# Kernel optimization log

Measured on AMD Instinct MI355X. Metric: run time of the kernel, lower is better.

## Reference

```python
import jax, jax.numpy as jnp
import numpy as np

B, D, U = 64, 256, 256

def setup_inputs() -> dict:
    key = jax.random.key(0)
    ks = jax.random.split(key, 16)
    init_mu = 0.05
    inputs = jax.random.normal(ks[0], (B, D), jnp.float32)
    prev_state = 0.1 * jax.random.normal(ks[1], (B, U), jnp.float32)
    A = jax.random.normal(ks[2], (B, U, U), jnp.float32)
    # symmetric, diagonally boosted covariance-like state
    Sigma_state = 0.01 * (A + jnp.swapaxes(A, 1, 2)) + 0.1 * jnp.eye(U, dtype=jnp.float32)
    def w(k, shape):
        return init_mu * jax.random.normal(k, shape, jnp.float32)
    def s(k):
        return jax.random.uniform(k, (U,), jnp.float32, -4.5, -2.2)
    return {
        'inputs': inputs, 'prev_state': prev_state, 'Sigma_state': Sigma_state,
        'U_z': w(ks[3], (D, U)), 'uz_sigma': s(ks[4]), 'W_z': w(ks[5], (U, U)), 'wz_sigma': s(ks[6]),
        'U_r': w(ks[7], (D, U)), 'ur_sigma': s(ks[8]), 'W_r': w(ks[9], (U, U)), 'wr_sigma': s(ks[10]),
        'U_h': w(ks[11], (D, U)), 'uh_sigma': s(ks[12]), 'W_h': w(ks[13], (U, U)), 'wh_sigma': s(ks[14]),
    }

def _outer(a, b):  # [B,u],[B,u] -> [B,u,u]
    return a[:, :, None] * b[:, None, :]

def _quad(W, S):  # W^T @ S @ W, S is [B,u,u]
    return jnp.matmul(jnp.matmul(W.T, S), W)

def _x_sigma_w(x, sv):  # ||x||^2 * diag(softplus sigma)
    return jnp.sum(x * x, axis=1)[:, None, None] * jnp.diag(sv)

def _tr_sigma_w(S, sv):  # trace(S) * diag(softplus sigma)
    return jnp.trace(S, axis1=1, axis2=2)[:, None, None] * jnp.diag(sv)

def _hadamard_sigma(S1, S2, m1, m2):
    # S1*S2 + diag(m1) S2 diag(m1) + diag(m2) S1 diag(m2) as elementwise/broadcast
    return S1 * S2 + _outer(m1, m1) * S2 + _outer(m2, m2) * S1

def reference(inputs, prev_state, Sigma_state, U_z, uz_sigma, W_z, wz_sigma,
              U_r, ur_sigma, W_r, wr_sigma, U_h, uh_sigma, W_h, wh_sigma):
    sp = jax.nn.softplus
    # --- z gate ---
    az = inputs @ U_z + prev_state @ W_z
    z = jax.nn.sigmoid(az)
    gz = z * (1.0 - z)  # d sigmoid
    Sz = (_quad(W_z, Sigma_state) + _x_sigma_w(prev_state, sp(wz_sigma))
          + _tr_sigma_w(Sigma_state, sp(wz_sigma)) + _x_sigma_w(inputs, sp(uz_sigma)))
    Sigma_out_z = Sz * _outer(gz, gz)
    # --- r gate ---
    ar = inputs @ U_r + prev_state @ W_r
    r = jax.nn.sigmoid(ar)
    gr = r * (1.0 - r)
    Sr = (_quad(W_r, Sigma_state) + _x_sigma_w(prev_state, sp(wr_sigma))
          + _tr_sigma_w(Sigma_state, sp(wr_sigma)) + _x_sigma_w(inputs, sp(ur_sigma)))
    Sigma_out_r = Sr * _outer(gr, gr)
    # --- h candidate ---
    g_in = prev_state * r
    ah = inputs @ U_h + g_in @ W_h
    h = jnp.tanh(ah)
    gh = 1.0 - h * h  # d tanh
    sigma_g = _hadamard_sigma(Sigma_state, Sigma_out_r, prev_state, r)
    Sh = (_quad(W_h, sigma_g) + _x_sigma_w(g_in, sp(wh_sigma))
          + _tr_sigma_w(sigma_g, sp(wh_sigma)) + _x_sigma_w(inputs, sp(uh_sigma)))
    Sigma_out_h = Sh * _outer(gh, gh)
    # --- output combination ---
    mu_out = z * prev_state + (1.0 - z) * h
    sigma_a = _hadamard_sigma(Sigma_out_z, Sigma_state, z, prev_state)
    sigma_b = _hadamard_sigma(Sigma_out_z, Sigma_out_h, 1.0 - z, h)
    Sigma_out = (sigma_a + sigma_b
                 - Sigma_out_z * _outer(prev_state, h)
                 - Sigma_out_z * _outer(h, prev_state))
    Sigma_out = jnp.where(jnp.isnan(Sigma_out) | jnp.isinf(Sigma_out),
                          jnp.zeros_like(Sigma_out), Sigma_out)
    eye = jnp.eye(Sigma_out.shape[-1], dtype=Sigma_out.dtype)
    d = jnp.abs(jnp.diagonal(Sigma_out, axis1=1, axis2=2))
    Sigma_out = Sigma_out * (1.0 - eye) + d[:, :, None] * eye
    return mu_out, Sigma_out
```

## Files before the change

kernel.cpp:

```cpp
#include <hip/hip_runtime.h>
#include <math.h>

#define UDIM 256
#define BATCH 64
#define MATN 65536
#define PITCH 280

typedef __bf16 bf16x8 __attribute__((ext_vector_type(8)));
typedef float  f32x4  __attribute__((ext_vector_type(4)));

__device__ __forceinline__ float softplusf(float x) { return log1pf(expf(x)); }
__device__ __forceinline__ float sigmoidf_(float x) { return 1.f/(1.f+expf(-x)); }

__device__ __forceinline__ bf16x8 frag_load(const __bf16* base, int rt, int kt, int lane) {
  return *(const bf16x8*)(base + (((size_t)(rt*8 + kt))*64 + lane)*8);
}

__device__ __forceinline__ bf16x8 cvt8(const float* p) {
  const float4 f0 = *(const float4*)p;
  const float4 f1 = *(const float4*)(p + 4);
  bf16x8 v;
  v[0]=(__bf16)f0.x; v[1]=(__bf16)f0.y; v[2]=(__bf16)f0.z; v[3]=(__bf16)f0.w;
  v[4]=(__bf16)f1.x; v[5]=(__bf16)f1.y; v[6]=(__bf16)f1.z; v[7]=(__bf16)f1.w;
  return v;
}

#define MFMA16 __builtin_amdgcn_mfma_f32_16x16x32_bf16

__global__ __launch_bounds__(256) void prep_all(
    const float* __restrict__ Uz, const float* __restrict__ Wz,
    const float* __restrict__ Ur, const float* __restrict__ Wr,
    const float* __restrict__ Uh, const float* __restrict__ Wh,
    __bf16* __restrict__ Fw_z, __bf16* __restrict__ Fw_r,
    __bf16* __restrict__ Fu_h, __bf16* __restrict__ Fw_h,
    const float* __restrict__ S, const float* __restrict__ x,
    const float* __restrict__ prev, float* __restrict__ scal,
    __bf16* __restrict__ Sf,
    float* __restrict__ zb, float* __restrict__ rb,
    float* __restrict__ gzb, float* __restrict__ grb,
    float* __restrict__ gin)
{
  const int bid = blockIdx.x;
  const int t = threadIdx.x;
  const int w = t >> 6, l = t & 63, r = l & 15, q = l >> 4;

  __shared__ __align__(16) unsigned char LDSU[16896];

  if (bid < 1024) {
    const int c = bid;
    const int bx = c & 3, by = (c >> 2) & 3, b = c >> 4;
    const size_t sb = (size_t)b * MATN;
#pragma unroll
    for (int ss = 0; ss < 2; ++ss) {
      const int s = t + ss*256;
      const int chunk = s >> 6, lane = s & 63;
      const int rt_l = chunk >> 1, kt_l = chunk & 1;
      const int row = by*64 + rt_l*16 + (lane & 15);
      const int col = bx*64 + kt_l*32 + (lane >> 4)*8;
      const bf16x8 v = cvt8(S + sb + (size_t)row*UDIM + col);
      *(bf16x8*)(Sf + sb + (((size_t)((by*4 + rt_l)*8 + bx*2 + kt_l))*64 + lane)*8) = v;
    }
    return;
  }

  if (bid < 1088) {
    const int u3 = bid - 1024;
    const int mat = u3 >> 4, tl = u3 & 15;
    const int n0 = (tl & 3)*64, k0 = (tl >> 2)*64;
    const float* W; __bf16* F;
    switch (mat) {
      case 0: W = Wz; F = Fw_z; break;  case 1: W = Wr; F = Fw_r; break;
      case 2: W = Uh; F = Fu_h; break;  default: W = Wh; F = Fw_h; break;
    }
    float (*tile)[65] = (float (*)[65])LDSU;
    const int tx = t & 15, ty = t >> 4;
#pragma unroll
    for (int rr = 0; rr < 4; ++rr) {
      const int row = ty*4 + rr;
      const float4 f = *(const float4*)(W + (size_t)(k0 + row)*UDIM + n0 + tx*4);
      tile[row][tx*4+0] = f.x; tile[row][tx*4+1] = f.y;
      tile[row][tx*4+2] = f.z; tile[row][tx*4+3] = f.w;
    }
    __syncthreads();
#pragma unroll
    for (int ss = 0; ss < 2; ++ss) {
      const int s = t + ss*256;
      const int rt_l = s >> 7, kt_l = (s >> 6) & 1, lane = s & 63;
      const int nl = rt_l*16 + (lane & 15), kb = kt_l*32 + (lane >> 4)*8;
      __align__(16) __bf16 tmp[8];
#pragma unroll
      for (int e = 0; e < 8; ++e) tmp[e] = (__bf16)tile[kb + e][nl];
      *(uint4*)(F + (((size_t)((((n0 >> 4) + rt_l)*8) + (k0 >> 5) + kt_l))*64 + lane)*8)
          = *(const uint4*)tmp;
    }
    return;
  }

  if (bid < 1104) {
    const int blk = bid - 1088;
    const int b0 = blk*4 + (t >> 6);
    const float4 xv = *(const float4*)(x + b0*UDIM + l*4);
    float s0 = xv.x*xv.x + xv.y*xv.y + xv.z*xv.z + xv.w*xv.w;
    const float4 pv = *(const float4*)(prev + b0*UDIM + l*4);
    float s1 = pv.x*pv.x + pv.y*pv.y + pv.z*pv.z + pv.w*pv.w;
    float s2 = 0.f;
#pragma unroll
    for (int e = 0; e < 4; ++e)
      s2 += S[(size_t)b0*MATN + (size_t)(l*4 + e)*257];
    for (int off = 32; off; off >>= 1) {
      s0 += __shfl_down(s0, off);
      s1 += __shfl_down(s1, off);
      s2 += __shfl_down(s2, off);
    }
    if (l == 0) { scal[b0] = s0; scal[64 + b0] = s1; scal[128 + b0] = s2; }
    return;
  }

  {
    const int u2 = bid - 1104;
    const int g = u2 >> 4, un = u2 & 15;
    const int n0 = un * 16;
    const float* Um = g ? Ur : Uz;
    const float* Wm = g ? Wr : Wz;
    __bf16 (*Ut)[16][264] = (__bf16 (*)[16][264])LDSU;
    {
      float uv[16], wv[16];
      const float* ur_ = Um + (size_t)t*UDIM + n0;
      const float* wr_ = Wm + (size_t)t*UDIM + n0;
#pragma unroll
      for (int p4 = 0; p4 < 4; ++p4) {
        *(float4*)&uv[p4*4] = *(const float4*)(ur_ + p4*4);
        *(float4*)&wv[p4*4] = *(const float4*)(wr_ + p4*4);
      }
#pragma unroll
      for (int e = 0; e < 16; ++e) {
        Ut[0][e][t] = (__bf16)uv[e];
        Ut[1][e][t] = (__bf16)wv[e];
      }
    }
    __syncthreads();

    const int mrow = w*16 + r;
    f32x4 acc = {};
#pragma unroll
    for (int ks = 0; ks < 16; ++ks) {
      const int k0 = ks*32;
      const float* asrc;
      int src, koff;
      if (k0 < 256) { asrc = x    + (size_t)mrow*UDIM + k0         + q*8; src = 0; koff = k0; }
      else          { asrc = prev + (size_t)mrow*UDIM + (k0 - 256) + q*8; src = 1; koff = k0 - 256; }
      const bf16x8 af = cvt8(asrc);
      const bf16x8 bv = *(const bf16x8*)&Ut[src][r][koff + q*8];
      acc = MFMA16(af, bv, acc, 0, 0, 0);
    }
    const int n = n0 + r;
    if (g == 0) {
#pragma unroll
      for (int v = 0; v < 4; ++v) {
        const int m = w*16 + q*4 + v;
        const float zv = sigmoidf_(acc[v]);
        zb[m*UDIM + n]  = zv;
        gzb[m*UDIM + n] = zv * (1.f - zv);
      }
    } else {
      float ggp[4];
#pragma unroll
      for (int v = 0; v < 4; ++v) {
        const int m = w*16 + q*4 + v;
        const float rv = sigmoidf_(acc[v]);
        const float pv = prev[m*UDIM + n];
        const float g2 = pv * rv;
        rb[m*UDIM + n]  = rv;
        grb[m*UDIM + n] = rv * (1.f - rv);
        gin[m*UDIM + n] = g2;
        ggp[v] = g2 * g2;
      }
#pragma unroll
      for (int s2 = 1; s2 < 16; s2 <<= 1)
#pragma unroll
        for (int v = 0; v < 4; ++v) ggp[v] += __shfl_xor(ggp[v], s2);
      if (r == 0)
#pragma unroll
        for (int v = 0; v < 4; ++v)
          atomicAdd(&scal[192 + w*16 + q*4 + v], ggp[v]);
    }
  }
}

__global__ __launch_bounds__(256, 4) void quad_zr_gh(
    const float* __restrict__ S, const __bf16* __restrict__ Sf,
    const float* __restrict__ prev,
    const float* __restrict__ rb, const float* __restrict__ gzb,
    const float* __restrict__ grb,
    const float* __restrict__ wz_s, const float* __restrict__ uz_s,
    const float* __restrict__ wr_s, const float* __restrict__ ur_s,
    const __bf16* __restrict__ Fw_z, const __bf16* __restrict__ Fw_r,
    float* __restrict__ scal, __bf16* __restrict__ Szb, __bf16* __restrict__ G,
    const float* __restrict__ x, const float* __restrict__ gin,
    const float* __restrict__ zb,
    const __bf16* __restrict__ Fu_h, const __bf16* __restrict__ Fw_h,
    float* __restrict__ hb, float* __restrict__ ghb, float* __restrict__ mu_out)
{
  const int bid = blockIdx.x;
  const int t = threadIdx.x, w = t >> 6, l = t & 63, r = l & 15, q = l >> 4;

  if (bid < 4) {
    const int jt = bid;
    const int mrow = w*16 + r;
    f32x4 acc[4] = {};
#pragma unroll
    for (int ks = 0; ks < 16; ++ks) {
      const int k0 = ks*32;
      const float* asrc; const __bf16* B; int kk;
      if (k0 < 256) { asrc = x   + (size_t)mrow*UDIM + k0         + q*8; B = Fu_h; kk = k0; }
      else          { asrc = gin + (size_t)mrow*UDIM + (k0 - 256) + q*8; B = Fw_h; kk = k0 - 256; }
      const bf16x8 af = cvt8(asrc);
#pragma unroll
      for (int ni = 0; ni < 4; ++ni) {
        const bf16x8 bv = frag_load(B, jt*4 + ni, kk >> 5, l);
        acc[ni] = MFMA16(af, bv, acc[ni], 0, 0, 0);
      }
    }
#pragma unroll
    for (int ni = 0; ni < 4; ++ni) {
      const int n = jt*64 + ni*16 + r;
#pragma unroll
      for (int v = 0; v < 4; ++v) {
        const int m = w*16 + q*4 + v;
        const float hv = tanhf(acc[ni][v]);
        const float zv = zb[m*UDIM + n];
        hb[m*UDIM + n]  = hv;
        ghb[m*UDIM + n] = 1.f - hv*hv;
        mu_out[m*UDIM + n] = zv * prev[m*UDIM + n] + (1.f - zv) * hv;
      }
    }
    return;
  }

  const int id = bid - 4;
  const int s = id >> 6, b = id & 63;
  const size_t sb = (size_t)b * MATN;
  const __bf16* Sfb = Sf + sb;

  __shared__ __align__(16) __bf16 T[2*16*PITCH];
  __bf16* Tz = T;
  __bf16* Tr = T + 16*PITCH;

  f32x4 az[4] = {}, ar[4] = {};
#pragma unroll
  for (int kp = 0; kp < 4; ++kp) {
    bf16x8 wzf[2], wrf[2], sv[2][4];
#pragma unroll
    for (int u = 0; u < 2; ++u) {
      const int kt = kp*2 + u;
      wzf[u] = frag_load(Fw_z, s, kt, l);
      wrf[u] = frag_load(Fw_r, s, kt, l);
#pragma unroll
      for (int ct = 0; ct < 4; ++ct) sv[u][ct] = frag_load(Sfb, w*4 + ct, kt, l);
    }
#pragma unroll
    for (int u = 0; u < 2; ++u)
#pragma unroll
      for (int ct = 0; ct < 4; ++ct) {
        az[ct] = MFMA16(wzf[u], sv[u][ct], az[ct], 0, 0, 0);
        ar[ct] = MFMA16(wrf[u], sv[u][ct], ar[ct], 0, 0, 0);
      }
  }
#pragma unroll
  for (int ct = 0; ct < 4; ++ct)
#pragma unroll
    for (int v = 0; v < 4; ++v) {
      Tz[(q*4 + v)*PITCH + w*64 + ct*16 + r] = (__bf16)az[ct][v];
      Tr[(q*4 + v)*PITCH + w*64 + ct*16 + r] = (__bf16)ar[ct][v];
    }
  __syncthreads();

  const int ib = s*16 + q*4;
  const f32x4 gz4 = *(const f32x4*)(gzb + b*UDIM + ib);
  const f32x4 gr4 = *(const f32x4*)(grb + b*UDIM + ib);
  const f32x4 pp4 = *(const f32x4*)(prev + b*UDIM + ib);
  const f32x4 rr4 = *(const f32x4*)(rb + b*UDIM + ib);
  float Sv[16];
#pragma unroll
  for (int ct = 0; ct < 4; ++ct)
#pragma unroll
    for (int v = 0; v < 4; ++v)
      Sv[ct*4 + v] = S[sb + (size_t)(ib + v)*UDIM + (w*4 + ct)*16 + r];
  const float xx = scal[b];
  const float dscal = scal[64 + b] + scal[128 + b];

  f32x4 qz[4] = {}, qr[4] = {};
#pragma unroll
  for (int kt = 0; kt < 8; ++kt) {
    bf16x8 bwz[4], bwr[4];
#pragma unroll
    for (int ct = 0; ct < 4; ++ct) {
      bwz[ct] = frag_load(Fw_z, w*4 + ct, kt, l);
      bwr[ct] = frag_load(Fw_r, w*4 + ct, kt, l);
    }
    const bf16x8 atz = *(const bf16x8*)&Tz[r*PITCH + kt*32 + q*8];
    const bf16x8 atr = *(const bf16x8*)&Tr[r*PITCH + kt*32 + q*8];
#pragma unroll
    for (int ct = 0; ct < 4; ++ct) {
      qz[ct] = MFMA16(atz, bwz[ct], qz[ct], 0, 0, 0);
      qr[ct] = MFMA16(atr, bwr[ct], qr[ct], 0, 0, 0);
    }
  }

  {
    __align__(16) __bf16 o16[16];
#pragma unroll
    for (int ct = 0; ct < 4; ++ct) {
      const int j = (w*4 + ct)*16 + r;
      const float gj = gzb[b*UDIM + j];
#pragma unroll
      for (int v = 0; v < 4; ++v) {
        const int i = ib + v;
        float qv = qz[ct][v];
        if (i == j) qv += dscal*softplusf(wz_s[i]) + xx*softplusf(uz_s[i]);
        o16[ct*4 + v] = (__bf16)(qv * gz4[v] * gj);
      }
    }
    __bf16* dst = Szb + ((size_t)(b*16 + s)*256 + t)*16;
    *(uint4*)dst       = *(const uint4*)&o16[0];
    *(uint4*)(dst + 8) = *(const uint4*)&o16[8];
  }

  {
    float gvals[16];
    float trg = 0.f;
#pragma unroll
    for (int ct = 0; ct < 4; ++ct) {
      const int j = (w*4 + ct)*16 + r;
      const float gj = grb[b*UDIM + j];
      const float pj = prev[b*UDIM + j];
      const float rj = rb[b*UDIM + j];
#pragma unroll
      for (int v = 0; v < 4; ++v) {
        const int i = ib + v;
        float qv = qr[ct][v];
        if (i == j) qv += dscal*softplusf(wr_s[i]) + xx*softplusf(ur_s[i]);
        const float Sg = qv * gr4[v] * gj;
        const float sv = Sv[ct*4 + v];
        const float go = Sg*(sv + pp4[v]*pj) + rr4[v]*rj*sv;
        gvals[ct*4 + v] = go;
        if (i == j) trg += go;
      }
    }
    if (trg != 0.f) atomicAdd(&scal[256 + b], trg);

    __syncthreads();
#pragma unroll
    for (int ct = 0; ct < 4; ++ct)
#pragma unroll
      for (int v = 0; v < 4; ++v)
        Tr[(q*4 + v)*PITCH + w*64 + ct*16 + r] = (__bf16)gvals[ct*4 + v];
    __syncthreads();
#pragma unroll
    for (int ee = 0; ee < 2; ++ee) {
      const int e = t + ee*256;
      const int kt = e >> 6, le = e & 63;
      const uint4 vv = *(const uint4*)&Tr[(le & 15)*PITCH + kt*32 + (le >> 4)*8];
      *(uint4*)(G + sb + (((size_t)(s*8 + kt))*64 + le)*8) = vv;
    }
  }
}

__global__ __launch_bounds__(256, 4) void quad_h(
    const float* __restrict__ S, const __bf16* __restrict__ Szb,
    const float* __restrict__ prev, const float* __restrict__ zb,
    const float* __restrict__ hb, const float* __restrict__ ghb,
    const float* __restrict__ wh_s, const float* __restrict__ uh_s,
    const __bf16* __restrict__ Fw_h, const __bf16* __restrict__ G,
    const float* __restrict__ scal, float* __restrict__ out_sig)
{
  const int bid = blockIdx.x;
  const int s = bid >> 6, b = bid & 63;
  const size_t sb = (size_t)b * MATN;
  const int t = threadIdx.x, w = t >> 6, l = t & 63, r = l & 15, q = l >> 4;
  const __bf16* Gb = G + sb;

  __shared__ __align__(16) __bf16 Th[16*PITCH];

  f32x4 ah[4] = {};
#pragma unroll
  for (int kp = 0; kp < 4; ++kp) {
    bf16x8 af[2], bv[2][4];
#pragma unroll
    for (int u = 0; u < 2; ++u) {
      const int kt = kp*2 + u;
      af[u] = frag_load(Fw_h, s, kt, l);
#pragma unroll
      for (int ct = 0; ct < 4; ++ct) bv[u][ct] = frag_load(Gb, w*4 + ct, kt, l);
    }
#pragma unroll
    for (int u = 0; u < 2; ++u)
#pragma unroll
      for (int ct = 0; ct < 4; ++ct)
        ah[ct] = MFMA16(af[u], bv[u][ct], ah[ct], 0, 0, 0);
  }
#pragma unroll
  for (int ct = 0; ct < 4; ++ct)
#pragma unroll
    for (int v = 0; v < 4; ++v)
      Th[(q*4 + v)*PITCH + w*64 + ct*16 + r] = (__bf16)ah[ct][v];
  __syncthreads();

  const int ib = s*16 + q*4;
  const __bf16* szp = Szb + ((size_t)(b*16 + s)*256 + t)*16;
  __align__(16) __bf16 sz16[16];
  *(uint4*)&sz16[0] = *(const uint4*)szp;
  *(uint4*)&sz16[8] = *(const uint4*)(szp + 8);
  const f32x4 g4 = *(const f32x4*)(ghb + b*UDIM + ib);
  const f32x4 p4 = *(const f32x4*)(prev + b*UDIM + ib);
  const f32x4 z4 = *(const f32x4*)(zb + b*UDIM + ib);
  const f32x4 h4 = *(const f32x4*)(hb + b*UDIM + ib);
  float Sv[16], gjv[4], pjv[4], zjv[4], hjv[4];
#pragma unroll
  for (int ct = 0; ct < 4; ++ct) {
    const int j = (w*4 + ct)*16 + r;
    gjv[ct] = ghb[b*UDIM + j];
    pjv[ct] = prev[b*UDIM + j];
    zjv[ct] = zb[b*UDIM + j];
    hjv[ct] = hb[b*UDIM + j];
#pragma unroll
    for (int v = 0; v < 4; ++v)
      Sv[ct*4 + v] = S[sb + (size_t)(ib + v)*UDIM + j];
  }
  const float xx = scal[b];
  const float dscal = scal[192 + b] + scal[256 + b];

  f32x4 qh[4] = {};
#pragma unroll
  for (int kt = 0; kt < 8; ++kt) {
    bf16x8 bw[4];
#pragma unroll
    for (int ct = 0; ct < 4; ++ct) bw[ct] = frag_load(Fw_h, w*4 + ct, kt, l);
    const bf16x8 at = *(const bf16x8*)&Th[r*PITCH + kt*32 + q*8];
#pragma unroll
    for (int ct = 0; ct < 4; ++ct)
      qh[ct] = MFMA16(at, bw[ct], qh[ct], 0, 0, 0);
  }

#pragma unroll
  for (int ct = 0; ct < 4; ++ct) {
    const int j = (w*4 + ct)*16 + r;
#pragma unroll
    for (int v = 0; v < 4; ++v) {
      const int i = ib + v;
      float qv = qh[ct][v];
      if (i == j) qv += dscal*softplusf(wh_s[i]) + xx*softplusf(uh_s[i]);
      const float Sg = qv * g4[v] * gjv[ct];
      const float sv = Sv[ct*4 + v];
      const float sz = (float)sz16[ct*4 + v];
      float val = sv*(sz + z4[v]*zjv[ct])
                + sz*(p4[v] - h4[v])*(pjv[ct] - hjv[ct])
                + Sg*(sz + (1.f - z4[v])*(1.f - zjv[ct]));
      if (!isfinite(val)) val = 0.f;
      if (i == j) val = fabsf(val);
      out_sig[sb + (size_t)i*UDIM + j] = val;
    }
  }
}

extern "C" void kernel_launch(void* const* d_in, const int* in_sizes, int n_in,
                              void* d_out, int out_size, void* d_ws, size_t ws_size,
                              hipStream_t stream) {
  const float* x    = (const float*)d_in[0];
  const float* prev = (const float*)d_in[1];
  const float* S    = (const float*)d_in[2];
  const float* Uz   = (const float*)d_in[3];
  const float* uz_s = (const float*)d_in[4];
  const float* Wz   = (const float*)d_in[5];
  const float* wz_s = (const float*)d_in[6];
  const float* Ur   = (const float*)d_in[7];
  const float* ur_s = (const float*)d_in[8];
  const float* Wr   = (const float*)d_in[9];
  const float* wr_s = (const float*)d_in[10];
  const float* Uh   = (const float*)d_in[11];
  const float* uh_s = (const float*)d_in[12];
  const float* Wh   = (const float*)d_in[13];
  const float* wh_s = (const float*)d_in[14];

  float* out_mu  = (float*)d_out;
  float* out_sig = out_mu + BATCH*UDIM;

  float* ws   = (float*)d_ws;
  float* zb   = ws;
  float* rb   = zb  + BATCH*UDIM;
  float* gzb  = rb  + BATCH*UDIM;
  float* grb  = gzb + BATCH*UDIM;
  float* gin  = grb + BATCH*UDIM;
  float* hb   = gin + BATCH*UDIM;
  float* ghb  = hb  + BATCH*UDIM;
  float* scal = ghb + BATCH*UDIM;
  __bf16* bws  = (__bf16*)(scal + 512);
  __bf16* Fw_z = bws;
  __bf16* Fw_r = Fw_z + MATN;
  __bf16* Fu_h = Fw_r + MATN;
  __bf16* Fw_h = Fu_h + MATN;
  const size_t BIG = (size_t)BATCH * MATN;
  __bf16* Szb = Fw_h + MATN;
  __bf16* G   = Szb + BIG;
  __bf16* Sf  = G + BIG;

  (void)hipMemsetAsync(scal, 0, 512*sizeof(float), stream);

  prep_all<<<dim3(1136), 256, 0, stream>>>(Uz, Wz, Ur, Wr, Uh, Wh,
      Fw_z, Fw_r, Fu_h, Fw_h, S, x, prev, scal, Sf,
      zb, rb, gzb, grb, gin);
  quad_zr_gh<<<dim3(1028), 256, 0, stream>>>(S, Sf, prev, rb, gzb, grb,
      wz_s, uz_s, wr_s, ur_s, Fw_z, Fw_r, scal, Szb, G,
      x, gin, zb, Fu_h, Fw_h, hb, ghb, out_mu);
  quad_h<<<dim3(1024), 256, 0, stream>>>(S, Szb, prev, zb, hb, ghb,
      wh_s, uh_s, Fw_h, G, scal, out_sig);
}
```

Before: 164.2 us.

## Fuse z/r and h quadratic kernels with per-batch atomic counter barrier

Merges the z/r-gate quadratic kernel and the h-gate quadratic kernel into one launch. The 16 row-slab blocks of each batch synchronise through a global atomic counter spin-wait, and the h-candidate GEMM work is spread across 16 blocks that signal a separate counter. This keeps the z-gate covariance slab in registers instead of writing and re-reading an Szb bf16 buffer, and reuses the already loaded S values and prev. It removes one kernel launch and a large intermediate round trip, but relies on all 1024 blocks being co-resident to avoid deadlock and adds spin-wait stalls.

```diff
diff --git a/kernel.cpp b/kernel.cpp
--- a/kernel.cpp
+++ b/kernel.cpp
@@ -187,64 +187,67 @@
   }
 }
 
-__global__ __launch_bounds__(256, 4) void quad_zr_gh(
+__global__ __launch_bounds__(256, 4) void quad_all(
     const float* __restrict__ S, const __bf16* __restrict__ Sf,
     const float* __restrict__ prev,
     const float* __restrict__ rb, const float* __restrict__ gzb,
     const float* __restrict__ grb,
     const float* __restrict__ wz_s, const float* __restrict__ uz_s,
     const float* __restrict__ wr_s, const float* __restrict__ ur_s,
+    const float* __restrict__ wh_s, const float* __restrict__ uh_s,
     const __bf16* __restrict__ Fw_z, const __bf16* __restrict__ Fw_r,
-    float* __restrict__ scal, __bf16* __restrict__ Szb, __bf16* __restrict__ G,
+    const __bf16* __restrict__ Fu_h, const __bf16* __restrict__ Fw_h,
+    float* __restrict__ scal, unsigned int* __restrict__ cnt,
+    __bf16* __restrict__ G,
     const float* __restrict__ x, const float* __restrict__ gin,
     const float* __restrict__ zb,
-    const __bf16* __restrict__ Fu_h, const __bf16* __restrict__ Fw_h,
-    float* __restrict__ hb, float* __restrict__ ghb, float* __restrict__ mu_out)
+    float* __restrict__ hb, float* __restrict__ ghb,
+    float* __restrict__ mu_out, float* __restrict__ out_sig)
 {
   const int bid = blockIdx.x;
+  const int s = bid >> 6, b = bid & 63;
   const int t = threadIdx.x, w = t >> 6, l = t & 63, r = l & 15, q = l >> 4;
-
-  if (bid < 4) {
-    const int jt = bid;
-    const int mrow = w*16 + r;
-    f32x4 acc[4] = {};
-#pragma unroll
-    for (int ks = 0; ks < 16; ++ks) {
-      const int k0 = ks*32;
-      const float* asrc; const __bf16* B; int kk;
-      if (k0 < 256) { asrc = x   + (size_t)mrow*UDIM + k0         + q*8; B = Fu_h; kk = k0; }
-      else          { asrc = gin + (size_t)mrow*UDIM + (k0 - 256) + q*8; B = Fw_h; kk = k0 - 256; }
-      const bf16x8 af = cvt8(asrc);
-#pragma unroll
-      for (int ni = 0; ni < 4; ++ni) {
-        const bf16x8 bv = frag_load(B, jt*4 + ni, kk >> 5, l);
-        acc[ni] = MFMA16(af, bv, acc[ni], 0, 0, 0);
-      }
-    }
-#pragma unroll
-    for (int ni = 0; ni < 4; ++ni) {
-      const int n = jt*64 + ni*16 + r;
-#pragma unroll
-      for (int v = 0; v < 4; ++v) {
-        const int m = w*16 + q*4 + v;
-        const float hv = tanhf(acc[ni][v]);
-        const float zv = zb[m*UDIM + n];
-        hb[m*UDIM + n]  = hv;
-        ghb[m*UDIM + n] = 1.f - hv*hv;
-        mu_out[m*UDIM + n] = zv * prev[m*UDIM + n] + (1.f - zv) * hv;
-      }
-    }
-    return;
-  }
-
-  const int id = bid - 4;
-  const int s = id >> 6, b = id & 63;
   const size_t sb = (size_t)b * MATN;
   const __bf16* Sfb = Sf + sb;
 
   __shared__ __align__(16) __bf16 T[2*16*PITCH];
   __bf16* Tz = T;
   __bf16* Tr = T + 16*PITCH;
+
+  if (s == 15 && b >= 48) {
+    const int un = b - 48;
+    const int mrow = w*16 + r;
+    f32x4 acc = {};
+#pragma unroll
+    for (int kq = 0; kq < 4; ++kq) {
+      bf16x8 af[4], bv[4];
+#pragma unroll
+      for (int u = 0; u < 4; ++u) {
+        const int k0 = (kq*4 + u)*32;
+        if (k0 < 256) {
+          af[u] = cvt8(x   + (size_t)mrow*UDIM + k0 + q*8);
+          bv[u] = frag_load(Fu_h, un, k0 >> 5, l);
+        } else {
+          af[u] = cvt8(gin + (size_t)mrow*UDIM + (k0 - 256) + q*8);
+          bv[u] = frag_load(Fw_h, un, (k0 - 256) >> 5, l);
+        }
+      }
+#pragma unroll
+      for (int u = 0; u < 4; ++u) acc = MFMA16(af[u], bv[u], acc, 0, 0, 0);
+    }
+    const int n = un*16 + r;
+#pragma unroll
+    for (int v = 0; v < 4; ++v) {
+      const int m = w*16 + q*4 + v;
+      const float hv = tanhf(acc[v]);
+      const float zv = zb[m*UDIM + n];
+      hb[m*UDIM + n]  = hv;
+      ghb[m*UDIM + n] = 1.f - hv*hv;
+      mu_out[m*UDIM + n] = zv * prev[m*UDIM + n] + (1.f - zv) * hv;
+    }
+    __syncthreads();
+    if (t == 0) { __threadfence(); atomicAdd(&cnt[64], 1u); }
+  }
 
   f32x4 az[4] = {}, ar[4] = {};
 #pragma unroll
@@ -280,12 +283,15 @@
   const f32x4 gr4 = *(const f32x4*)(grb + b*UDIM + ib);
   const f32x4 pp4 = *(const f32x4*)(prev + b*UDIM + ib);
   const f32x4 rr4 = *(const f32x4*)(rb + b*UDIM + ib);
-  float Sv[16];
-#pragma unroll
-  for (int ct = 0; ct < 4; ++ct)
+  float Sv[16], pjv[4];
+#pragma unroll
+  for (int ct = 0; ct < 4; ++ct) {
+    const int j = (w*4 + ct)*16 + r;
+    pjv[ct] = prev[b*UDIM + j];
 #pragma unroll
     for (int v = 0; v < 4; ++v)
-      Sv[ct*4 + v] = S[sb + (size_t)(ib + v)*UDIM + (w*4 + ct)*16 + r];
+      Sv[ct*4 + v] = S[sb + (size_t)(ib + v)*UDIM + j];
+  }
   const float xx = scal[b];
   const float dscal = scal[64 + b] + scal[128 + b];
 
@@ -307,23 +313,18 @@
     }
   }
 
-  {
-    __align__(16) __bf16 o16[16];
-#pragma unroll
-    for (int ct = 0; ct < 4; ++ct) {
-      const int j = (w*4 + ct)*16 + r;
-      const float gj = gzb[b*UDIM + j];
-#pragma unroll
-      for (int v = 0; v < 4; ++v) {
-        const int i = ib + v;
-        float qv = qz[ct][v];
-        if (i == j) qv += dscal*softplusf(wz_s[i]) + xx*softplusf(uz_s[i]);
-        o16[ct*4 + v] = (__bf16)(qv * gz4[v] * gj);
-      }
-    }
-    __bf16* dst = Szb + ((size_t)(b*16 + s)*256 + t)*16;
-    *(uint4*)dst       = *(const uint4*)&o16[0];
-    *(uint4*)(dst + 8) = *(const uint4*)&o16[8];
+  __align__(16) __bf16 o16[16];
+#pragma unroll
+  for (int ct = 0; ct < 4; ++ct) {
+    const int j = (w*4 + ct)*16 + r;
+    const float gj = gzb[b*UDIM + j];
+#pragma unroll
+    for (int v = 0; v < 4; ++v) {
+      const int i = ib + v;
+      float qv = qz[ct][v];
+      if (i == j) qv += dscal*softplusf(wz_s[i]) + xx*softplusf(uz_s[i]);
+      o16[ct*4 + v] = (__bf16)(qv * gz4[v] * gj);
+    }
   }
 
   {
@@ -333,7 +334,6 @@
     for (int ct = 0; ct < 4; ++ct) {
       const int j = (w*4 + ct)*16 + r;
       const float gj = grb[b*UDIM + j];
-      const float pj = prev[b*UDIM + j];
       const float rj = rb[b*UDIM + j];
 #pragma unroll
       for (int v = 0; v < 4; ++v) {
@@ -342,7 +342,7 @@
         if (i == j) qv += dscal*softplusf(wr_s[i]) + xx*softplusf(ur_s[i]);
         const float Sg = qv * gr4[v] * gj;
         const float sv = Sv[ct*4 + v];
-        const float go = Sg*(sv + pp4[v]*pj) + rr4[v]*rj*sv;
+        const float go = Sg*(sv + pp4[v]*pjv[ct]) + rr4[v]*rj*sv;
         gvals[ct*4 + v] = go;
         if (i == j) trg += go;
       }
@@ -364,101 +364,89 @@
       *(uint4*)(G + sb + (((size_t)(s*8 + kt))*64 + le)*8) = vv;
     }
   }
-}
-
-__global__ __launch_bounds__(256, 4) void quad_h(
-    const float* __restrict__ S, const __bf16* __restrict__ Szb,
-    const float* __restrict__ prev, const float* __restrict__ zb,
-    const float* __restrict__ hb, const float* __restrict__ ghb,
-    const float* __restrict__ wh_s, const float* __restrict__ uh_s,
-    const __bf16* __restrict__ Fw_h, const __bf16* __restrict__ G,
-    const float* __restrict__ scal, float* __restrict__ out_sig)
-{
-  const int bid = blockIdx.x;
-  const int s = bid >> 6, b = bid & 63;
-  const size_t sb = (size_t)b * MATN;
-  const int t = threadIdx.x, w = t >> 6, l = t & 63, r = l & 15, q = l >> 4;
-  const __bf16* Gb = G + sb;
-
-  __shared__ __align__(16) __bf16 Th[16*PITCH];
-
-  f32x4 ah[4] = {};
-#pragma unroll
-  for (int kp = 0; kp < 4; ++kp) {
-    bf16x8 af[2], bv[2][4];
-#pragma unroll
-    for (int u = 0; u < 2; ++u) {
-      const int kt = kp*2 + u;
-      af[u] = frag_load(Fw_h, s, kt, l);
-#pragma unroll
-      for (int ct = 0; ct < 4; ++ct) bv[u][ct] = frag_load(Gb, w*4 + ct, kt, l);
-    }
-#pragma unroll
-    for (int u = 0; u < 2; ++u)
+
+  __syncthreads();
+  if (t == 0) {
+    __threadfence();
+    atomicAdd(&cnt[b], 1u);
+    while (__hip_atomic_load(&cnt[b], __ATOMIC_RELAXED, __HIP_MEMORY_SCOPE_AGENT) < 16u
+        || __hip_atomic_load(&cnt[64], __ATOMIC_RELAXED, __HIP_MEMORY_SCOPE_AGENT) < 16u)
+      __builtin_amdgcn_s_sleep(2);
+    __threadfence();
+  }
+  __syncthreads();
+
+  {
+    const __bf16* Gb = G + sb;
+    __bf16* Th = T;
+
+    f32x4 ah[4] = {};
+#pragma unroll
+    for (int kp = 0; kp < 4; ++kp) {
+      bf16x8 af[2], bv[2][4];
+#pragma unroll
+      for (int u = 0; u < 2; ++u) {
+        const int kt = kp*2 + u;
+        af[u] = frag_load(Fw_h, s, kt, l);
+#pragma unroll
+        for (int ct = 0; ct < 4; ++ct) bv[u][ct] = frag_load(Gb, w*4 + ct, kt, l);
+      }
+#pragma unroll
+      for (int u = 0; u < 2; ++u)
+#pragma unroll
+        for (int ct = 0; ct < 4; ++ct)
+          ah[ct] = MFMA16(af[u], bv[u][ct], ah[ct], 0, 0, 0);
+    }
+#pragma unroll
+    for (int ct = 0; ct < 4; ++ct)
+#pragma unroll
+      for (int v = 0; v < 4; ++v)
+        Th[(q*4 + v)*PITCH + w*64 + ct*16 + r] = (__bf16)ah[ct][v];
+    __syncthreads();
+
+    const f32x4 g4 = *(const f32x4*)(ghb + b*UDIM + ib);
+    const f32x4 z4 = *(const f32x4*)(zb + b*UDIM + ib);
+    const f32x4 h4 = *(const f32x4*)(hb + b*UDIM + ib);
+    float gjv[4], zjv[4], hjv[4];
+#pragma unroll
+    for (int ct = 0; ct < 4; ++ct) {
+      const int j = (w*4 + ct)*16 + r;
+      gjv[ct] = ghb[b*UDIM + j];
+      zjv[ct] = zb[b*UDIM + j];
+      hjv[ct] = hb[b*UDIM + j];
+    }
+    const float dsch = scal[192 + b] + scal[256 + b];
+
+    f32x4 qh[4] = {};
+#pragma unroll
+    for (int kt = 0; kt < 8; ++kt) {
+      bf16x8 bw[4];
+#pragma unroll
+      for (int ct = 0; ct < 4; ++ct) bw[ct] = frag_load(Fw_h, w*4 + ct, kt, l);
+      const bf16x8 at = *(const bf16x8*)&Th[r*PITCH + kt*32 + q*8];
 #pragma unroll
       for (int ct = 0; ct < 4; ++ct)
-        ah[ct] = MFMA16(af[u], bv[u][ct], ah[ct], 0, 0, 0);
-  }
-#pragma unroll
-  for (int ct = 0; ct < 4; ++ct)
-#pragma unroll
-    for (int v = 0; v < 4; ++v)
-      Th[(q*4 + v)*PITCH + w*64 + ct*16 + r] = (__bf16)ah[ct][v];
-  __syncthreads();
-
-  const int ib = s*16 + q*4;
-  const __bf16* szp = Szb + ((size_t)(b*16 + s)*256 + t)*16;
-  __align__(16) __bf16 sz16[16];
-  *(uint4*)&sz16[0] = *(const uint4*)szp;
-  *(uint4*)&sz16[8] = *(const uint4*)(szp + 8);
-  const f32x4 g4 = *(const f32x4*)(ghb + b*UDIM + ib);
-  const f32x4 p4 = *(const f32x4*)(prev + b*UDIM + ib);
-  const f32x4 z4 = *(const f32x4*)(zb + b*UDIM + ib);
-  const f32x4 h4 = *(const f32x4*)(hb + b*UDIM + ib);
-  float Sv[16], gjv[4], pjv[4], zjv[4], hjv[4];
-#pragma unroll
-  for (int ct = 0; ct < 4; ++ct) {
-    const int j = (w*4 + ct)*16 + r;
-    gjv[ct] = ghb[b*UDIM + j];
-    pjv[ct] = prev[b*UDIM + j];
-    zjv[ct] = zb[b*UDIM + j];
-    hjv[ct] = hb[b*UDIM + j];
-#pragma unroll
-    for (int v = 0; v < 4; ++v)
-      Sv[ct*4 + v] = S[sb + (size_t)(ib + v)*UDIM + j];
-  }
-  const float xx = scal[b];
-  const float dscal = scal[192 + b] + scal[256 + b];
-
-  f32x4 qh[4] = {};
-#pragma unroll
-  for (int kt = 0; kt < 8; ++kt) {
-    bf16x8 bw[4];
-#pragma unroll
-    for (int ct = 0; ct < 4; ++ct) bw[ct] = frag_load(Fw_h, w*4 + ct, kt, l);
-    const bf16x8 at = *(const bf16x8*)&Th[r*PITCH + kt*32 + q*8];
-#pragma unroll
-    for (int ct = 0; ct < 4; ++ct)
-      qh[ct] = MFMA16(at, bw[ct], qh[ct], 0, 0, 0);
-  }
-
-#pragma unroll
-  for (int ct = 0; ct < 4; ++ct) {
-    const int j = (w*4 + ct)*16 + r;
-#pragma unroll
-    for (int v = 0; v < 4; ++v) {
-      const int i = ib + v;
-      float qv = qh[ct][v];
-      if (i == j) qv += dscal*softplusf(wh_s[i]) + xx*softplusf(uh_s[i]);
-      const float Sg = qv * g4[v] * gjv[ct];
-      const float sv = Sv[ct*4 + v];
-      const float sz = (float)sz16[ct*4 + v];
-      float val = sv*(sz + z4[v]*zjv[ct])
-                + sz*(p4[v] - h4[v])*(pjv[ct] - hjv[ct])
-                + Sg*(sz + (1.f - z4[v])*(1.f - zjv[ct]));
-      if (!isfinite(val)) val = 0.f;
-      if (i == j) val = fabsf(val);
-      out_sig[sb + (size_t)i*UDIM + j] = val;
+        qh[ct] = MFMA16(at, bw[ct], qh[ct], 0, 0, 0);
+    }
+
+#pragma unroll
+    for (int ct = 0; ct < 4; ++ct) {
+      const int j = (w*4 + ct)*16 + r;
+#pragma unroll
+      for (int v = 0; v < 4; ++v) {
+        const int i = ib + v;
+        float qv = qh[ct][v];
+        if (i == j) qv += dsch*softplusf(wh_s[i]) + xx*softplusf(uh_s[i]);
+        const float Sg = qv * g4[v] * gjv[ct];
+        const float sv = Sv[ct*4 + v];
+        const float sz = (float)o16[ct*4 + v];
+        float val = sv*(sz + z4[v]*zjv[ct])
+                  + sz*(pp4[v] - h4[v])*(pjv[ct] - hjv[ct])
+                  + Sg*(sz + (1.f - z4[v])*(1.f - zjv[ct]));
+        if (!isfinite(val)) val = 0.f;
+        if (i == j) val = fabsf(val);
+        out_sig[sb + (size_t)i*UDIM + j] = val;
+      }
     }
   }
 }
@@ -494,24 +482,23 @@
   float* hb   = gin + BATCH*UDIM;
   float* ghb  = hb  + BATCH*UDIM;
   float* scal = ghb + BATCH*UDIM;
-  __bf16* bws  = (__bf16*)(scal + 512);
+  unsigned int* cnt = (unsigned int*)(scal + 512);
+  __bf16* bws  = (__bf16*)(scal + 512 + 80);
   __bf16* Fw_z = bws;
   __bf16* Fw_r = Fw_z + MATN;
   __bf16* Fu_h = Fw_r + MATN;
   __bf16* Fw_h = Fu_h + MATN;
   const size_t BIG = (size_t)BATCH * MATN;
-  __bf16* Szb = Fw_h + MATN;
-  __bf16* G   = Szb + BIG;
+  __bf16* G   = Fw_h + MATN;
   __bf16* Sf  = G + BIG;
 
-  (void)hipMemsetAsync(scal, 0, 512*sizeof(float), stream);
+  (void)hipMemsetAsync(scal, 0, (512 + 80)*sizeof(float), stream);
 
   prep_all<<<dim3(1136), 256, 0, stream>>>(Uz, Wz, Ur, Wr, Uh, Wh,
       Fw_z, Fw_r, Fu_h, Fw_h, S, x, prev, scal, Sf,
       zb, rb, gzb, grb, gin);
-  quad_zr_gh<<<dim3(1028), 256, 0, stream>>>(S, Sf, prev, rb, gzb, grb,
-      wz_s, uz_s, wr_s, ur_s, Fw_z, Fw_r, scal, Szb, G,
-      x, gin, zb, Fu_h, Fw_h, hb, ghb, out_mu);
-  quad_h<<<dim3(1024), 256, 0, stream>>>(S, Szb, prev, zb, hb, ghb,
-      wh_s, uh_s, Fw_h, G, scal, out_sig);
+  quad_all<<<dim3(1024), 256, 0, stream>>>(S, Sf, prev, rb, gzb, grb,
+      wz_s, uz_s, wr_s, ur_s, wh_s, uh_s,
+      Fw_z, Fw_r, Fu_h, Fw_h, scal, cnt, G,
+      x, gin, zb, hb, ghb, out_mu, out_sig);
 }
```

New measurement: 284.3 us. +73.1%, slower.

## Replace atomics with per-slot partial sums and drop scalar memset launch

Applied to the files above, without the earlier changes.

Global atomicAdd accumulations for the gin-squared norms and the trace of sigma_g now go into dedicated per-tile slots in the scratch buffer, and the consumer kernel sums those slots itself. This removes the hipMemsetAsync launch, since every slot is overwritten each call. The prep blocks for weights, norms and gates are folded into the first 112 of the 1024 S-conversion blocks, and the gh/mu blocks are folded into the last four quad blocks, so the launch grids shrink. The blocks that take on extra work become longer, which can leave a tail at the end of each launch.

```diff
diff --git a/kernel.cpp b/kernel.cpp
--- a/kernel.cpp
+++ b/kernel.cpp
@@ -5,6 +5,8 @@
 #define BATCH 64
 #define MATN 65536
 #define PITCH 280
+#define GG_BASE 256
+#define TRG_BASE 1280
 
 typedef __bf16 bf16x8 __attribute__((ext_vector_type(8)));
 typedef float  f32x4  __attribute__((ext_vector_type(4)));
@@ -46,26 +48,8 @@
 
   __shared__ __align__(16) unsigned char LDSU[16896];
 
-  if (bid < 1024) {
-    const int c = bid;
-    const int bx = c & 3, by = (c >> 2) & 3, b = c >> 4;
-    const size_t sb = (size_t)b * MATN;
-#pragma unroll
-    for (int ss = 0; ss < 2; ++ss) {
-      const int s = t + ss*256;
-      const int chunk = s >> 6, lane = s & 63;
-      const int rt_l = chunk >> 1, kt_l = chunk & 1;
-      const int row = by*64 + rt_l*16 + (lane & 15);
-      const int col = bx*64 + kt_l*32 + (lane >> 4)*8;
-      const bf16x8 v = cvt8(S + sb + (size_t)row*UDIM + col);
-      *(bf16x8*)(Sf + sb + (((size_t)((by*4 + rt_l)*8 + bx*2 + kt_l))*64 + lane)*8) = v;
-    }
-    return;
-  }
-
-  if (bid < 1088) {
-    const int u3 = bid - 1024;
-    const int mat = u3 >> 4, tl = u3 & 15;
+  if (bid < 64) {
+    const int mat = bid >> 4, tl = bid & 15;
     const int n0 = (tl & 3)*64, k0 = (tl >> 2)*64;
     const float* W; __bf16* F;
     switch (mat) {
@@ -93,11 +77,8 @@
       *(uint4*)(F + (((size_t)((((n0 >> 4) + rt_l)*8) + (k0 >> 5) + kt_l))*64 + lane)*8)
           = *(const uint4*)tmp;
     }
-    return;
-  }
-
-  if (bid < 1104) {
-    const int blk = bid - 1088;
+  } else if (bid < 80) {
+    const int blk = bid - 64;
     const int b0 = blk*4 + (t >> 6);
     const float4 xv = *(const float4*)(x + b0*UDIM + l*4);
     float s0 = xv.x*xv.x + xv.y*xv.y + xv.z*xv.z + xv.w*xv.w;
@@ -113,11 +94,8 @@
       s2 += __shfl_down(s2, off);
     }
     if (l == 0) { scal[b0] = s0; scal[64 + b0] = s1; scal[128 + b0] = s2; }
-    return;
-  }
-
-  {
-    const int u2 = bid - 1104;
+  } else if (bid < 112) {
+    const int u2 = bid - 80;
     const int g = u2 >> 4, un = u2 & 15;
     const int n0 = un * 16;
     const float* Um = g ? Ur : Uz;
@@ -182,7 +160,23 @@
       if (r == 0)
 #pragma unroll
         for (int v = 0; v < 4; ++v)
-          atomicAdd(&scal[192 + w*16 + q*4 + v], ggp[v]);
+          scal[GG_BASE + (w*16 + q*4 + v)*16 + un] = ggp[v];
+    }
+  }
+
+  {
+    const int c = bid;
+    const int bx = c & 3, by = (c >> 2) & 3, b = c >> 4;
+    const size_t sb = (size_t)b * MATN;
+#pragma unroll
+    for (int ss = 0; ss < 2; ++ss) {
+      const int s = t + ss*256;
+      const int chunk = s >> 6, lane = s & 63;
+      const int rt_l = chunk >> 1, kt_l = chunk & 1;
+      const int row = by*64 + rt_l*16 + (lane & 15);
+      const int col = bx*64 + kt_l*32 + (lane >> 4)*8;
+      const bf16x8 v = cvt8(S + sb + (size_t)row*UDIM + col);
+      *(bf16x8*)(Sf + sb + (((size_t)((by*4 + rt_l)*8 + bx*2 + kt_l))*64 + lane)*8) = v;
     }
   }
 }
@@ -203,9 +197,15 @@
 {
   const int bid = blockIdx.x;
   const int t = threadIdx.x, w = t >> 6, l = t & 63, r = l & 15, q = l >> 4;
-
-  if (bid < 4) {
-    const int jt = bid;
+  const int s = bid >> 6, b = bid & 63;
+
+  __shared__ __align__(16) __bf16 T[2*16*PITCH];
+  __shared__ float red4[4];
+  __bf16* Tz = T;
+  __bf16* Tr = T + 16*PITCH;
+
+  if (bid >= 1020) {
+    const int jt = bid - 1020;
     const int mrow = w*16 + r;
     f32x4 acc[4] = {};
 #pragma unroll
@@ -234,17 +234,10 @@
         mu_out[m*UDIM + n] = zv * prev[m*UDIM + n] + (1.f - zv) * hv;
       }
     }
-    return;
-  }
-
-  const int id = bid - 4;
-  const int s = id >> 6, b = id & 63;
+  }
+
   const size_t sb = (size_t)b * MATN;
   const __bf16* Sfb = Sf + sb;
-
-  __shared__ __align__(16) __bf16 T[2*16*PITCH];
-  __bf16* Tz = T;
-  __bf16* Tr = T + 16*PITCH;
 
   f32x4 az[4] = {}, ar[4] = {};
 #pragma unroll
@@ -347,9 +340,12 @@
         if (i == j) trg += go;
       }
     }
-    if (trg != 0.f) atomicAdd(&scal[256 + b], trg);
+    for (int off = 32; off; off >>= 1) trg += __shfl_down(trg, off);
+    if (l == 0) red4[w] = trg;
 
     __syncthreads();
+    if (t == 0)
+      scal[TRG_BASE + b*16 + s] = red4[0] + red4[1] + red4[2] + red4[3];
 #pragma unroll
     for (int ct = 0; ct < 4; ++ct)
 #pragma unroll
@@ -428,7 +424,13 @@
       Sv[ct*4 + v] = S[sb + (size_t)(ib + v)*UDIM + j];
   }
   const float xx = scal[b];
-  const float dscal = scal[192 + b] + scal[256 + b];
+  float dscal = 0.f;
+#pragma unroll
+  for (int e = 0; e < 4; ++e) {
+    const f32x4 a = *(const f32x4*)(scal + GG_BASE + b*16 + e*4);
+    const f32x4 c = *(const f32x4*)(scal + TRG_BASE + b*16 + e*4);
+    dscal += a[0]+a[1]+a[2]+a[3] + c[0]+c[1]+c[2]+c[3];
+  }
 
   f32x4 qh[4] = {};
 #pragma unroll
@@ -494,7 +496,7 @@
   float* hb   = gin + BATCH*UDIM;
   float* ghb  = hb  + BATCH*UDIM;
   float* scal = ghb + BATCH*UDIM;
-  __bf16* bws  = (__bf16*)(scal + 512);
+  __bf16* bws  = (__bf16*)(scal + 2304);
   __bf16* Fw_z = bws;
   __bf16* Fw_r = Fw_z + MATN;
   __bf16* Fu_h = Fw_r + MATN;
@@ -504,12 +506,10 @@
   __bf16* G   = Szb + BIG;
   __bf16* Sf  = G + BIG;
 
-  (void)hipMemsetAsync(scal, 0, 512*sizeof(float), stream);
-
-  prep_all<<<dim3(1136), 256, 0, stream>>>(Uz, Wz, Ur, Wr, Uh, Wh,
+  prep_all<<<dim3(1024), 256, 0, stream>>>(Uz, Wz, Ur, Wr, Uh, Wh,
       Fw_z, Fw_r, Fu_h, Fw_h, S, x, prev, scal, Sf,
       zb, rb, gzb, grb, gin);
-  quad_zr_gh<<<dim3(1028), 256, 0, stream>>>(S, Sf, prev, rb, gzb, grb,
+  quad_zr_gh<<<dim3(1024), 256, 0, stream>>>(S, Sf, prev, rb, gzb, grb,
       wz_s, uz_s, wr_s, ur_s, Fw_z, Fw_r, scal, Szb, G,
       x, gin, zb, Fu_h, Fw_h, hb, ghb, out_mu);
   quad_h<<<dim3(1024), 256, 0, stream>>>(S, Szb, prev, zb, hb, ghb,
```

Result: no change. 162.6 us (-1.0%).
